# Performance work log

Measured on AMD Instinct MI355X. Metric: run time of the kernel, lower is better.

Reference implementation:

```python
import jax, jax.numpy as jnp
import numpy as np

N, C, H, W = 512, 512, 14, 14
CH, CW = 7, 7  # RoIAlign crop size


def conv1x1(x, w, b):
    # x: [N,C,H,W], w: [O,C], b: [O]  (1x1 conv == channel GEMM)
    return jnp.einsum('nchw,oc->nohw', x, w) + b[None, :, None, None]


def roi_align_fpcoor(x, boxes, ch, cw):
    """RoIAlign(transform_fpcoor=True) as in longcw/RoIAlign.pytorch.
    x: [N,C,H,W]; boxes: [N,4] = (x1,y1,x2,y2) in feature-pixel coords,
    box n crops image n. Returns [N,C,ch,cw]."""
    Hf, Wf = x.shape[2], x.shape[3]
    x1, y1, x2, y2 = boxes[:, 0], boxes[:, 1], boxes[:, 2], boxes[:, 3]
    sw = (x2 - x1) / cw
    sh = (y2 - y1) / ch
    nx0 = (x1 + sw * 0.5 - 0.5) / (Wf - 1)
    ny0 = (y1 + sh * 0.5 - 0.5) / (Hf - 1)
    nw = sw * (cw - 1) / (Wf - 1)
    nh = sh * (ch - 1) / (Hf - 1)
    # tf.crop_and_resize sample coordinates (crop size > 1 branch)
    ys = ny0[:, None] * (Hf - 1) + jnp.arange(ch, dtype=x.dtype) * (nh[:, None] * (Hf - 1) / (ch - 1))  # [N,ch]
    xs = nx0[:, None] * (Wf - 1) + jnp.arange(cw, dtype=x.dtype) * (nw[:, None] * (Wf - 1) / (cw - 1))  # [N,cw]
    y0f = jnp.floor(ys); x0f = jnp.floor(xs)
    wy = (ys - y0f)[:, :, None, None]          # [N,ch,1,1]
    wx = (xs - x0f)[:, None, :, None]          # [N,1,cw,1]
    y0 = jnp.clip(y0f.astype(jnp.int32), 0, Hf - 1)
    y1i = jnp.clip(y0 + 1, 0, Hf - 1)
    x0 = jnp.clip(x0f.astype(jnp.int32), 0, Wf - 1)
    x1i = jnp.clip(x0 + 1, 0, Wf - 1)
    b = jnp.arange(x.shape[0])[:, None, None]  # [N,1,1]
    yA = y0[:, :, None]; yB = y1i[:, :, None]  # [N,ch,1]
    xA = x0[:, None, :]; xB = x1i[:, None, :]  # [N,1,cw]
    # advanced indexing -> [N,ch,cw,C]
    v00 = x[b, :, yA, xA]; v01 = x[b, :, yA, xB]
    v10 = x[b, :, yB, xA]; v11 = x[b, :, yB, xB]
    top = v00 + (v01 - v00) * wx
    bot = v10 + (v11 - v10) * wx
    out = top + (bot - top) * wy               # [N,ch,cw,C]
    return jnp.transpose(out, (0, 3, 1, 2))    # [N,C,ch,cw]


def setup_inputs() -> dict:
    key = jax.random.key(0)
    ks = jax.random.split(key, 11)
    s = 0.02
    d = C * CH * CW  # 512*49
    return {
        'project': jax.random.normal(ks[0], (N, C, H, W), jnp.float32),
        'w1': jax.random.normal(ks[1], (C, C), jnp.float32) * s,
        'b1': jnp.zeros((C,), jnp.float32),
        'w2': jax.random.normal(ks[2], (C, C), jnp.float32) * s,
        'b2': jnp.zeros((C,), jnp.float32),
        'w3': jax.random.normal(ks[3], (C, C), jnp.float32) * s,
        'b3': jnp.zeros((C,), jnp.float32),
        'w_note': jax.random.normal(ks[4], (2, d), jnp.float32) * s,
        'b_note': jnp.zeros((2,), jnp.float32),
        'w_reg': jax.random.normal(ks[5], (8, d), jnp.float32) * s,
        'b_reg': jnp.zeros((8,), jnp.float32),
    }


def reference(project, w1, b1, w2, b2, w3, b3, w_note, b_note, w_reg, b_reg):
    x = conv1x1(project, w1, b1)
    x = conv1x1(x, w2, b2)
    # boxes are a fixed constant inside forward: [0,0,13,13] per RoI
    boxes = jnp.tile(jnp.asarray([[0.0, 0.0, 13.0, 13.0]], jnp.float32), (project.shape[0], 1))
    x = roi_align_fpcoor(x, boxes, CH, CW)     # [N,512,7,7]
    x = conv1x1(x, w3, b3)
    x = x.reshape((-1, C * CH * CW))
    note = x @ w_note.T + b_note
    reg = x @ w_reg.T + b_reg
    return note, reg
```

## Files before the change

### kernel.cpp

```cpp
#include <hip/hip_runtime.h>


#define CHW4 25088
#define STEP 1.8571428571428572f

__global__ __launch_bounds__(512) void k_prep1(
    const float* __restrict__ w_note, const float* __restrict__ w_reg,
    const float* __restrict__ w2, const float* __restrict__ b1,
    const float* __restrict__ b2,
    float* __restrict__ WH, float* __restrict__ u2) {
    int blk = blockIdx.x;
    int tid = threadIdx.x;
    if (blk < 490) {
        int k = blk / 49, ji = blk % 49;
        const float* wh = (k < 2) ? (w_note + k * 25088) : (w_reg + (k - 2) * 25088);
        WH[(size_t)blk * 512 + tid] = wh[tid * 49 + ji];
    } else {
        int wv = tid >> 6, lane = tid & 63;
        int o = (blk - 490) * 8 + wv;
        float s = 0.f;
        #pragma unroll
        for (int r = 0; r < 8; ++r) s += w2[(size_t)o * 512 + lane + r * 64] * b1[lane + r * 64];
        for (int off = 32; off; off >>= 1) s += __shfl_down(s, off);
        if (lane == 0) u2[o] = b2[o] + s;
    }
}

__global__ __launch_bounds__(256) void k_prep2(
    const float* __restrict__ w1, const float* __restrict__ w2,
    const float* __restrict__ w3, const float* __restrict__ WH,
    const float* __restrict__ u2, const float* __restrict__ b3,
    float* __restrict__ Y, float* __restrict__ T1, float* __restrict__ vv) {
    int blk = blockIdx.x;
    int tid = threadIdx.x;
    if (blk < 512) {
        __shared__ float As[32][36];
        __shared__ float Bs[32][36];
        const float* A; const float* B; float* C; int M;
        if (blk < 256) { A = w2; B = w1; C = Y;  M = 512; }
        else           { A = WH; B = w3; C = T1; M = 490; }
        int t = blk & 255;
        int bx = t & 15, by = t >> 4;
        int lr = tid >> 3, lc = (tid & 7) << 2;
        int tx = tid & 15, ty = tid >> 4;
        float a00 = 0.f, a01 = 0.f, a10 = 0.f, a11 = 0.f;
        for (int kc = 0; kc < 512; kc += 32) {
            int gr = by * 32 + lr;
            float4 av = make_float4(0.f, 0.f, 0.f, 0.f);
            if (gr < M) av = *(const float4*)&A[(size_t)gr * 512 + kc + lc];
            *(float4*)&As[lr][lc] = av;
            *(float4*)&Bs[lr][lc] = *(const float4*)&B[(size_t)(kc + lr) * 512 + bx * 32 + lc];
            __syncthreads();
            #pragma unroll
            for (int kk = 0; kk < 32; ++kk) {
                float b0 = Bs[kk][tx * 2], b1v = Bs[kk][tx * 2 + 1];
                float x0 = As[ty * 2][kk], x1 = As[ty * 2 + 1][kk];
                a00 += x0 * b0; a01 += x0 * b1v;
                a10 += x1 * b0; a11 += x1 * b1v;
            }
            __syncthreads();
        }
        int r0 = by * 32 + ty * 2, c0 = bx * 32 + tx * 2;
        if (r0 < M)     { C[(size_t)r0 * 512 + c0] = a00; C[(size_t)r0 * 512 + c0 + 1] = a01; }
        if (r0 + 1 < M) { C[(size_t)(r0 + 1) * 512 + c0] = a10; C[(size_t)(r0 + 1) * 512 + c0 + 1] = a11; }
    } else {
        int wv = tid >> 6, lane = tid & 63;
        int o = (blk - 512) * 4 + wv;
        float s = 0.f;
        #pragma unroll
        for (int r = 0; r < 8; ++r) s += w3[(size_t)o * 512 + lane + r * 64] * u2[lane + r * 64];
        for (int off = 32; off; off >>= 1) s += __shfl_down(s, off);
        if (lane == 0) vv[o] = b3[o] + s;
    }
}

__global__ __launch_bounds__(256) void k_prep3(
    const float* __restrict__ T1, const float* __restrict__ Y,
    const float* __restrict__ w_note, const float* __restrict__ w_reg,
    const float* __restrict__ vv,
    float* __restrict__ Bmat, float* __restrict__ dpart) {
    int blk = blockIdx.x;
    int tid = threadIdx.x;
    if (blk < 256) {
        __shared__ float As[32][36];
        __shared__ float Bs[32][36];
        int bx = blk & 15, by = blk >> 4;
        int lr = tid >> 3, lc = (tid & 7) << 2;
        int tx = tid & 15, ty = tid >> 4;
        int gr = by * 32 + lr;
        float a00 = 0.f, a01 = 0.f, a10 = 0.f, a11 = 0.f;
        for (int kc = 0; kc < 512; kc += 32) {
            float4 av = make_float4(0.f, 0.f, 0.f, 0.f);
            if (gr < 490) av = *(const float4*)&T1[(size_t)gr * 512 + kc + lc];
            *(float4*)&As[lr][lc] = av;
            *(float4*)&Bs[lr][lc] = *(const float4*)&Y[(size_t)(kc + lr) * 512 + bx * 32 + lc];
            __syncthreads();
            #pragma unroll
            for (int kk = 0; kk < 32; ++kk) {
                float b0 = Bs[kk][tx * 2], b1v = Bs[kk][tx * 2 + 1];
                float x0 = As[ty * 2][kk], x1 = As[ty * 2 + 1][kk];
                a00 += x0 * b0; a01 += x0 * b1v;
                a10 += x1 * b0; a11 += x1 * b1v;
            }
            __syncthreads();
        }
        int r0 = by * 32 + ty * 2, c0 = bx * 32 + tx * 2;
        if (r0 < 490)     { Bmat[(size_t)r0 * 512 + c0] = a00; Bmat[(size_t)r0 * 512 + c0 + 1] = a01; }
        if (r0 + 1 < 490) { Bmat[(size_t)(r0 + 1) * 512 + c0] = a10; Bmat[(size_t)(r0 + 1) * 512 + c0 + 1] = a11; }
    } else {
        int t = blk - 256;
        int k = t >> 3, b8 = t & 7;
        const float* wh = (k < 2) ? (w_note + k * 25088) : (w_reg + (k - 2) * 25088);
        float s = 0.f;
        for (int i = b8 * 256 + tid; i < 25088; i += 2048) s += wh[i] * vv[i / 49];
        __shared__ float red[256];
        red[tid] = s;
        __syncthreads();
        for (int off = 128; off; off >>= 1) {
            if (tid < off) red[tid] += red[tid + off];
            __syncthreads();
        }
        if (tid == 0) dpart[k * 8 + b8] = red[0];
    }
}

__global__ __launch_bounds__(256) void k_mainf(const float* __restrict__ proj,
                                               const float* __restrict__ Bmat,
                                               float* __restrict__ part) {
    __shared__ float X[2][16][197];
    int b = blockIdx.x;
    int n = b >> 1;
    int ch0 = (b & 1) << 4;
    int tid = threadIdx.x;
    int wv = tid >> 6, lane = tid & 63;

    int cc0 = tid / 49,            q0 = tid - (tid / 49) * 49;
    int cc1 = cc0 + 5,             q1 = q0 + 11; if (q1 >= 49) { q1 -= 49; ++cc1; }
    int cc2 = cc1 + 5,             q2 = q1 + 11; if (q2 >= 49) { q2 -= 49; ++cc2; }

    const float base = STEP * 0.5f - 0.5f;
    int   i00s[4], bidx0s[4];
    float wxs[4], wys[4];
    #pragma unroll
    for (int s = 0; s < 4; ++s) {
        int o = tid + s * 256;
        if (o > 783) o = 783;
        int ji = o >> 4, cl = o & 15;
        int j = (ji * 37) >> 8;
        int i2 = ji - j * 7;
        float yv = base + j * STEP;
        float xv = base + i2 * STEP;
        float y0f = floorf(yv), x0f = floorf(xv);
        wys[s] = yv - y0f; wxs[s] = xv - x0f;
        i00s[s] = cl * 197 + (int)y0f * 14 + (int)x0f;
        bidx0s[s] = (ji << 9) + (ch0 << 4) + cl;
    }

    const float4* src0 = (const float4*)proj + (size_t)n * CHW4 + ch0 * 784;
    float acc[10];
    #pragma unroll
    for (int k = 0; k < 10; ++k) acc[k] = 0.f;

    {
        float4 v0 = src0[tid];
        float4 v1 = src0[tid + 256];
        float4 v2 = src0[tid + 512];
        float* xb = &X[0][0][0];
        *(float4*)&xb[cc0 * 197 + q0 * 4] = v0;
        *(float4*)&xb[cc1 * 197 + q1 * 4] = v1;
        *(float4*)&xb[cc2 * 197 + q2 * 4] = v2;
        if (tid < 16) *(float4*)&xb[15 * 197 + (tid + 33) * 4] = src0[tid + 768];
    }
    __syncthreads();

    int cur = 0;
    #pragma unroll 1
    for (int t = 0; t < 16; ++t) {
        float c0r[10], c1r[10], c2r[10], c3r[10];
        {
            const float* Bp0 = Bmat + bidx0s[0] + (t << 4);
            const float* Bp1 = Bmat + bidx0s[1] + (t << 4);
            const float* Bp2 = Bmat + bidx0s[2] + (t << 4);
            #pragma unroll
            for (int k = 0; k < 10; ++k) c0r[k] = Bp0[(size_t)k * 25088];
            #pragma unroll
            for (int k = 0; k < 10; ++k) c1r[k] = Bp1[(size_t)k * 25088];
            #pragma unroll
            for (int k = 0; k < 10; ++k) c2r[k] = Bp2[(size_t)k * 25088];
            if (tid < 16) {
                const float* Bp3 = Bmat + bidx0s[3] + (t << 4);
                #pragma unroll
                for (int k = 0; k < 10; ++k) c3r[k] = Bp3[(size_t)k * 25088];
            }
        }
        __builtin_amdgcn_sched_barrier(0);
        float4 v0, v1, v2, v3;
        if (t < 15) {
            const float4* sn = src0 + (t + 1) * 784;
            v0 = sn[tid]; v1 = sn[tid + 256]; v2 = sn[tid + 512];
            if (tid < 16) v3 = sn[tid + 768];
        }
        __builtin_amdgcn_sched_barrier(0);
        const float* xb = &X[cur][0][0];
        {
            int i00 = i00s[0];
            float v00 = xb[i00],      v01 = xb[i00 + 1];
            float v10 = xb[i00 + 14], v11 = xb[i00 + 15];
            float top = v00 + (v01 - v00) * wxs[0];
            float bot = v10 + (v11 - v10) * wxs[0];
            float v = top + (bot - top) * wys[0];
            #pragma unroll
            for (int k = 0; k < 10; ++k) acc[k] += v * c0r[k];
        }
        {
            int i00 = i00s[1];
            float v00 = xb[i00],      v01 = xb[i00 + 1];
            float v10 = xb[i00 + 14], v11 = xb[i00 + 15];
            float top = v00 + (v01 - v00) * wxs[1];
            float bot = v10 + (v11 - v10) * wxs[1];
            float v = top + (bot - top) * wys[1];
            #pragma unroll
            for (int k = 0; k < 10; ++k) acc[k] += v * c1r[k];
        }
        {
            int i00 = i00s[2];
            float v00 = xb[i00],      v01 = xb[i00 + 1];
            float v10 = xb[i00 + 14], v11 = xb[i00 + 15];
            float top = v00 + (v01 - v00) * wxs[2];
            float bot = v10 + (v11 - v10) * wxs[2];
            float v = top + (bot - top) * wys[2];
            #pragma unroll
            for (int k = 0; k < 10; ++k) acc[k] += v * c2r[k];
        }
        if (tid < 16) {
            int i00 = i00s[3];
            float v00 = xb[i00],      v01 = xb[i00 + 1];
            float v10 = xb[i00 + 14], v11 = xb[i00 + 15];
            float top = v00 + (v01 - v00) * wxs[3];
            float bot = v10 + (v11 - v10) * wxs[3];
            float v = top + (bot - top) * wys[3];
            #pragma unroll
            for (int k = 0; k < 10; ++k) acc[k] += v * c3r[k];
        }
        if (t < 15) {
            float* xw = &X[cur ^ 1][0][0];
            *(float4*)&xw[cc0 * 197 + q0 * 4] = v0;
            *(float4*)&xw[cc1 * 197 + q1 * 4] = v1;
            *(float4*)&xw[cc2 * 197 + q2 * 4] = v2;
            if (tid < 16) *(float4*)&xw[15 * 197 + (tid + 33) * 4] = v3;
        }
        __syncthreads();
        cur ^= 1;
    }

    #pragma unroll
    for (int k = 0; k < 10; ++k) {
        float v = acc[k];
        v += __shfl_xor(v, 1);
        v += __shfl_xor(v, 2);
        v += __shfl_xor(v, 4);
        v += __shfl_xor(v, 8);
        v += __shfl_xor(v, 16);
        v += __shfl_xor(v, 32);
        if (lane == k) part[((size_t)b * 4 + wv) * 10 + k] = v;
    }
}

__global__ void k_reduce(const float* __restrict__ part,
                         const float* __restrict__ dpart,
                         const float* __restrict__ b_note, const float* __restrict__ b_reg,
                         float* __restrict__ out) {
    int idx = blockIdx.x * 256 + threadIdx.x;
    int n = idx / 10, k = idx % 10;
    float s = (k < 2) ? b_note[k] : b_reg[k - 2];
    for (int b = 0; b < 8; ++b) s += dpart[k * 8 + b];
    #pragma unroll
    for (int h = 0; h < 2; ++h)
        for (int w = 0; w < 4; ++w)
            s += part[(((size_t)(n * 2 + h)) * 4 + w) * 10 + k];
    if (k < 2) out[n * 2 + k] = s;
    else       out[1024 + n * 8 + (k - 2)] = s;
}

extern "C" void kernel_launch(void* const* d_in, const int* in_sizes, int n_in,
                              void* d_out, int out_size, void* d_ws, size_t ws_size,
                              hipStream_t stream) {
    const float* proj   = (const float*)d_in[0];
    const float* w1     = (const float*)d_in[1];
    const float* b1     = (const float*)d_in[2];
    const float* w2     = (const float*)d_in[3];
    const float* b2     = (const float*)d_in[4];
    const float* w3     = (const float*)d_in[5];
    const float* b3     = (const float*)d_in[6];
    const float* w_note = (const float*)d_in[7];
    const float* b_note = (const float*)d_in[8];
    const float* w_reg  = (const float*)d_in[9];
    const float* b_reg  = (const float*)d_in[10];

    float* ws    = (float*)d_ws;
    float* WH    = ws;
    float* Y     = WH + 250880;
    float* T1    = Y + 262144;
    float* Bmat  = T1 + 250880;
    float* u2    = Bmat + 250880;
    float* vv    = u2 + 512;
    float* dpart = vv + 512;
    float* part  = dpart + 80;
    float* out   = (float*)d_out;

    k_prep1<<<554, 512, 0, stream>>>(w_note, w_reg, w2, b1, b2, WH, u2);
    k_prep2<<<640, 256, 0, stream>>>(w1, w2, w3, WH, u2, b3, Y, T1, vv);
    k_prep3<<<336, 256, 0, stream>>>(T1, Y, w_note, w_reg, vv, Bmat, dpart);
    k_mainf<<<1024, 256, 0, stream>>>(proj, Bmat, part);
    k_reduce<<<20, 256, 0, stream>>>(part, dpart, b_note, b_reg, out);
}
```

Baseline: 93.83 us.

## Process two images per block in main kernel to reuse Bmat coefficient loads

```diff
diff --git a/kernel.cpp b/kernel.cpp
--- a/kernel.cpp
+++ b/kernel.cpp
@@ -127,9 +127,9 @@
 __global__ __launch_bounds__(256) void k_mainf(const float* __restrict__ proj,
                                                const float* __restrict__ Bmat,
                                                float* __restrict__ part) {
-    __shared__ float X[2][16][197];
+    __shared__ float X[2][2][16][197];
     int b = blockIdx.x;
-    int n = b >> 1;
+    int np = b >> 1;
     int ch0 = (b & 1) << 4;
     int tid = threadIdx.x;
     int wv = tid >> 6, lane = tid & 63;
@@ -156,20 +156,29 @@
         bidx0s[s] = (ji << 9) + (ch0 << 4) + cl;
     }
 
-    const float4* src0 = (const float4*)proj + (size_t)n * CHW4 + ch0 * 784;
-    float acc[10];
+    const float4* srcA = (const float4*)proj + (size_t)(np * 2) * CHW4 + ch0 * 784;
+    const float4* srcB = srcA + CHW4;
+    float acc[2][10];
     #pragma unroll
-    for (int k = 0; k < 10; ++k) acc[k] = 0.f;
+    for (int j = 0; j < 2; ++j)
+        #pragma unroll
+        for (int k = 0; k < 10; ++k) acc[j][k] = 0.f;
 
     {
-        float4 v0 = src0[tid];
-        float4 v1 = src0[tid + 256];
-        float4 v2 = src0[tid + 512];
-        float* xb = &X[0][0][0];
-        *(float4*)&xb[cc0 * 197 + q0 * 4] = v0;
-        *(float4*)&xb[cc1 * 197 + q1 * 4] = v1;
-        *(float4*)&xb[cc2 * 197 + q2 * 4] = v2;
-        if (tid < 16) *(float4*)&xb[15 * 197 + (tid + 33) * 4] = src0[tid + 768];
+        float4 a0 = srcA[tid], a1 = srcA[tid + 256], a2 = srcA[tid + 512];
+        float4 b0 = srcB[tid], b1 = srcB[tid + 256], b2 = srcB[tid + 512];
+        float* xa = &X[0][0][0][0];
+        float* xb = &X[1][0][0][0];
+        *(float4*)&xa[cc0 * 197 + q0 * 4] = a0;
+        *(float4*)&xa[cc1 * 197 + q1 * 4] = a1;
+        *(float4*)&xa[cc2 * 197 + q2 * 4] = a2;
+        *(float4*)&xb[cc0 * 197 + q0 * 4] = b0;
+        *(float4*)&xb[cc1 * 197 + q1 * 4] = b1;
+        *(float4*)&xb[cc2 * 197 + q2 * 4] = b2;
+        if (tid < 16) {
+            *(float4*)&xa[15 * 197 + (tid + 33) * 4] = srcA[tid + 768];
+            *(float4*)&xb[15 * 197 + (tid + 33) * 4] = srcB[tid + 768];
+        }
     }
     __syncthreads();
 
@@ -194,76 +203,89 @@
             }
         }
         __builtin_amdgcn_sched_barrier(0);
-        float4 v0, v1, v2, v3;
+        float4 a0, a1, a2, a3, b0, b1, b2, b3;
         if (t < 15) {
-            const float4* sn = src0 + (t + 1) * 784;
-            v0 = sn[tid]; v1 = sn[tid + 256]; v2 = sn[tid + 512];
-            if (tid < 16) v3 = sn[tid + 768];
+            const float4* sa = srcA + (t + 1) * 784;
+            const float4* sb = srcB + (t + 1) * 784;
+            a0 = sa[tid]; a1 = sa[tid + 256]; a2 = sa[tid + 512];
+            b0 = sb[tid]; b1 = sb[tid + 256]; b2 = sb[tid + 512];
+            if (tid < 16) { a3 = sa[tid + 768]; b3 = sb[tid + 768]; }
         }
         __builtin_amdgcn_sched_barrier(0);
-        const float* xb = &X[cur][0][0];
-        {
-            int i00 = i00s[0];
-            float v00 = xb[i00],      v01 = xb[i00 + 1];
-            float v10 = xb[i00 + 14], v11 = xb[i00 + 15];
-            float top = v00 + (v01 - v00) * wxs[0];
-            float bot = v10 + (v11 - v10) * wxs[0];
-            float v = top + (bot - top) * wys[0];
-            #pragma unroll
-            for (int k = 0; k < 10; ++k) acc[k] += v * c0r[k];
-        }
-        {
-            int i00 = i00s[1];
-            float v00 = xb[i00],      v01 = xb[i00 + 1];
-            float v10 = xb[i00 + 14], v11 = xb[i00 + 15];
-            float top = v00 + (v01 - v00) * wxs[1];
-            float bot = v10 + (v11 - v10) * wxs[1];
-            float v = top + (bot - top) * wys[1];
-            #pragma unroll
-            for (int k = 0; k < 10; ++k) acc[k] += v * c1r[k];
-        }
-        {
-            int i00 = i00s[2];
-            float v00 = xb[i00],      v01 = xb[i00 + 1];
-            float v10 = xb[i00 + 14], v11 = xb[i00 + 15];
-            float top = v00 + (v01 - v00) * wxs[2];
-            float bot = v10 + (v11 - v10) * wxs[2];
-            float v = top + (bot - top) * wys[2];
-            #pragma unroll
-            for (int k = 0; k < 10; ++k) acc[k] += v * c2r[k];
+        const float* xa = &X[0][cur][0][0];
+        const float* xb = &X[1][cur][0][0];
+        #pragma unroll
+        for (int s = 0; s < 3; ++s) {
+            const float* cr = (s == 0) ? c0r : (s == 1) ? c1r : c2r;
+            int i00 = i00s[s];
+            float wxv = wxs[s], wyv = wys[s];
+            float va00 = xa[i00],      va01 = xa[i00 + 1];
+            float va10 = xa[i00 + 14], va11 = xa[i00 + 15];
+            float ta = va00 + (va01 - va00) * wxv;
+            float ba = va10 + (va11 - va10) * wxv;
+            float va = ta + (ba - ta) * wyv;
+            float vb00 = xb[i00],      vb01 = xb[i00 + 1];
+            float vb10 = xb[i00 + 14], vb11 = xb[i00 + 15];
+            float tb = vb00 + (vb01 - vb00) * wxv;
+            float bb = vb10 + (vb11 - vb10) * wxv;
+            float vb = tb + (bb - tb) * wyv;
+            #pragma unroll
+            for (int k = 0; k < 10; ++k) {
+                acc[0][k] += va * cr[k];
+                acc[1][k] += vb * cr[k];
+            }
         }
         if (tid < 16) {
             int i00 = i00s[3];
-            float v00 = xb[i00],      v01 = xb[i00 + 1];
-            float v10 = xb[i00 + 14], v11 = xb[i00 + 15];
-            float top = v00 + (v01 - v00) * wxs[3];
-            float bot = v10 + (v11 - v10) * wxs[3];
-            float v = top + (bot - top) * wys[3];
-            #pragma unroll
-            for (int k = 0; k < 10; ++k) acc[k] += v * c3r[k];
+            float wxv = wxs[3], wyv = wys[3];
+            float va00 = xa[i00],      va01 = xa[i00 + 1];
+            float va10 = xa[i00 + 14], va11 = xa[i00 + 15];
+            float ta = va00 + (va01 - va00) * wxv;
+            float ba = va10 + (va11 - va10) * wxv;
+            float va = ta + (ba - ta) * wyv;
+            float vb00 = xb[i00],      vb01 = xb[i00 + 1];
+            float vb10 = xb[i00 + 14], vb11 = xb[i00 + 15];
+            float tb = vb00 + (vb01 - vb00) * wxv;
+            float bb = vb10 + (vb11 - vb10) * wxv;
+            float vb = tb + (bb - tb) * wyv;
+            #pragma unroll
+            for (int k = 0; k < 10; ++k) {
+                acc[0][k] += va * c3r[k];
+                acc[1][k] += vb * c3r[k];
+            }
         }
         if (t < 15) {
-            float* xw = &X[cur ^ 1][0][0];
-            *(float4*)&xw[cc0 * 197 + q0 * 4] = v0;
-            *(float4*)&xw[cc1 * 197 + q1 * 4] = v1;
-            *(float4*)&xw[cc2 * 197 + q2 * 4] = v2;
-            if (tid < 16) *(float4*)&xw[15 * 197 + (tid + 33) * 4] = v3;
+            float* xwa = &X[0][cur ^ 1][0][0];
+            float* xwb = &X[1][cur ^ 1][0][0];
+            *(float4*)&xwa[cc0 * 197 + q0 * 4] = a0;
+            *(float4*)&xwa[cc1 * 197 + q1 * 4] = a1;
+            *(float4*)&xwa[cc2 * 197 + q2 * 4] = a2;
+            *(float4*)&xwb[cc0 * 197 + q0 * 4] = b0;
+            *(float4*)&xwb[cc1 * 197 + q1 * 4] = b1;
+            *(float4*)&xwb[cc2 * 197 + q2 * 4] = b2;
+            if (tid < 16) {
+                *(float4*)&xwa[15 * 197 + (tid + 33) * 4] = a3;
+                *(float4*)&xwb[15 * 197 + (tid + 33) * 4] = b3;
+            }
         }
         __syncthreads();
         cur ^= 1;
     }
 
     #pragma unroll
-    for (int k = 0; k < 10; ++k) {
-        float v = acc[k];
-        v += __shfl_xor(v, 1);
-        v += __shfl_xor(v, 2);
-        v += __shfl_xor(v, 4);
-        v += __shfl_xor(v, 8);
-        v += __shfl_xor(v, 16);
-        v += __shfl_xor(v, 32);
-        if (lane == k) part[((size_t)b * 4 + wv) * 10 + k] = v;
-    }
+    for (int j = 0; j < 2; ++j)
+        #pragma unroll
+        for (int k = 0; k < 10; ++k) {
+            float v = acc[j][k];
+            v += __shfl_xor(v, 1);
+            v += __shfl_xor(v, 2);
+            v += __shfl_xor(v, 4);
+            v += __shfl_xor(v, 8);
+            v += __shfl_xor(v, 16);
+            v += __shfl_xor(v, 32);
+            if (lane == j * 10 + k)
+                part[(((size_t)b * 4 + wv) * 2 + j) * 10 + k] = v;
+        }
 }
 
 __global__ void k_reduce(const float* __restrict__ part,
@@ -272,12 +294,13 @@
                          float* __restrict__ out) {
     int idx = blockIdx.x * 256 + threadIdx.x;
     int n = idx / 10, k = idx % 10;
+    int np = n >> 1, j = n & 1;
     float s = (k < 2) ? b_note[k] : b_reg[k - 2];
-    for (int b = 0; b < 8; ++b) s += dpart[k * 8 + b];
+    for (int b8 = 0; b8 < 8; ++b8) s += dpart[k * 8 + b8];
     #pragma unroll
     for (int h = 0; h < 2; ++h)
         for (int w = 0; w < 4; ++w)
-            s += part[(((size_t)(n * 2 + h)) * 4 + w) * 10 + k];
+            s += part[((((size_t)(np * 2 + h)) * 4 + w) * 2 + j) * 10 + k];
     if (k < 2) out[n * 2 + k] = s;
     else       out[1024 + n * 8 + (k - 2)] = s;
 }
@@ -311,6 +334,6 @@
     k_prep1<<<554, 512, 0, stream>>>(w_note, w_reg, w2, b1, b2, WH, u2);
     k_prep2<<<640, 256, 0, stream>>>(w1, w2, w3, WH, u2, b3, Y, T1, vv);
     k_prep3<<<336, 256, 0, stream>>>(T1, Y, w_note, w_reg, vv, Bmat, dpart);
-    k_mainf<<<1024, 256, 0, stream>>>(proj, Bmat, part);
+    k_mainf<<<512, 256, 0, stream>>>(proj, Bmat, part);
     k_reduce<<<20, 256, 0, stream>>>(part, dpart, b_note, b_reg, out);
 }
```

Measured after the change: 83.99 us, median of 2. 1.12x faster.
